# Kernel tuning notes

Measured on AMD Instinct MI355X. Metric: run time of the kernel, lower is better.

Reference implementation:

```python
import jax, jax.numpy as jnp
import numpy as np

HIDDEN, NOISE, MLPW, NCOND, DATA, INIT_NOISE = 64, 16, 128, 4, 8, 16
T, B = 128, 8192
TSCALE = 1.0


def _lipswish(x):
    return 0.909 * x * jax.nn.sigmoid(x)


def _mlp(x, Ws, bs):
    for W, b in zip(Ws[:-1], bs[:-1]):
        x = _lipswish(x @ W + b)
    return TSCALE * jnp.tanh(x @ Ws[-1] + bs[-1])  # tanh regularization, tscale=1.0


def setup_inputs():
    key = jax.random.key(0)
    ks = jax.random.split(key, 12)

    def lin(k, fi, fo):
        k1, k2 = jax.random.split(k)
        lim = 1.0 / float(np.sqrt(fi))
        W = jax.random.uniform(k1, (fi, fo), minval=-lim, maxval=lim, dtype=jnp.float32)
        b = jax.random.uniform(k2, (fo,), minval=-lim, maxval=lim, dtype=jnp.float32)
        return W, b

    ind = 1 + HIDDEN + NCOND  # cat([t, x, c0])
    dr_W0, dr_b0 = lin(ks[0], ind, MLPW)
    dr_W1, dr_b1 = lin(ks[1], MLPW, MLPW)
    dr_W2, dr_b2 = lin(ks[2], MLPW, HIDDEN)
    di_W0, di_b0 = lin(ks[3], ind, MLPW)
    di_W1, di_b1 = lin(ks[4], MLPW, MLPW)
    di_W2, di_b2 = lin(ks[5], MLPW, HIDDEN * NOISE)
    init_W, init_b = lin(ks[6], INIT_NOISE + NCOND, HIDDEN)
    ro_W, ro_b = lin(ks[7], HIDDEN + NCOND, DATA)

    ts = jnp.linspace(0.0, 1.0, T, dtype=jnp.float32)
    dt = 1.0 / (T - 1)
    dW = jax.random.normal(ks[8], (T - 1, B, NOISE), dtype=jnp.float32) * float(np.sqrt(dt))
    conditions = jax.random.normal(ks[9], (NCOND,), dtype=jnp.float32)
    return dict(ts=ts, conditions=conditions, dW=dW,
                dr_W0=dr_W0, dr_b0=dr_b0, dr_W1=dr_W1, dr_b1=dr_b1, dr_W2=dr_W2, dr_b2=dr_b2,
                di_W0=di_W0, di_b0=di_b0, di_W1=di_W1, di_b1=di_b1, di_W2=di_W2, di_b2=di_b2,
                init_W=init_W, init_b=init_b, ro_W=ro_W, ro_b=ro_b, batch_size=B)


def reference(ts, conditions, dW, dr_W0, dr_b0, dr_W1, dr_b1, dr_W2, dr_b2,
              di_W0, di_b0, di_W1, di_b1, di_W2, di_b2, init_W, init_b, ro_W, ro_b,
              batch_size):
    drWs, drbs = (dr_W0, dr_W1, dr_W2), (dr_b0, dr_b1, dr_b2)
    diWs, dibs = (di_W0, di_W1, di_W2), (di_b0, di_b1, di_b2)

    h0 = jnp.ones((batch_size, INIT_NOISE), jnp.float32)  # fixed=True initial point
    c0 = jnp.broadcast_to(conditions[None, :], (batch_size, NCOND))
    x0 = jnp.concatenate([h0, c0], 1) @ init_W + init_b  # (B, H)

    def fg(t, x):
        tcol = jnp.full((x.shape[0], 1), t, x.dtype)
        tx = jnp.concatenate([tcol, x, c0], 1)
        f = _mlp(tx, drWs, drbs)  # (B, H)
        g = _mlp(tx, diWs, dibs).reshape(x.shape[0], HIDDEN, NOISE)  # (B, H, M)
        return f, g

    f0, g0 = fg(ts[0], x0)
    dts = jnp.diff(ts)

    def step(carry, inp):
        y, z, fz, gz = carry
        t1, dt, dw = inp
        # reversible Heun (Stratonovich): auxiliary state z, re-used (f,g) at (t_n, z_n)
        z1 = 2.0 * y - z + fz * dt + jnp.einsum('bhm,bm->bh', gz, dw)
        f1, g1 = fg(t1, z1)
        y1 = y + 0.5 * dt * (fz + f1) + 0.5 * jnp.einsum('bhm,bm->bh', gz + g1, dw)
        return (y1, z1, f1, g1), y1

    _, ys = jax.lax.scan(step, (x0, x0, f0, g0), (ts[1:], dts, dW))
    xs = jnp.concatenate([x0[None], ys], 0).transpose(1, 0, 2)  # (B, T, H)
    nT = xs.shape[1]
    cs = jnp.broadcast_to(c0[:, None, :], (batch_size, nT, NCOND))
    out = jnp.concatenate([xs, cs], -1) @ ro_W + ro_b  # (B, T, data)
    ts_e = jnp.broadcast_to(ts[None, :, None], (batch_size, nT, 1))
    # linear_interpolation_coeffs with no NaNs is the identity on the values
    return jnp.concatenate([ts_e, out], -1)  # (B, T, 1 + data)
```

## Files before the change

kernel.cpp:

```cpp
#include <hip/hip_runtime.h>
#include <hip/hip_bf16.h>
#include <cstdint>
#include <cstddef>

#define B_TOT   8192
#define T_TOT   128
#define ROWS    32
#define THREADS 1024

typedef __bf16 bf16x8 __attribute__((ext_vector_type(8)));
typedef float  f32x4  __attribute__((ext_vector_type(4)));

#define WSF_X0    0
#define WSF_BCD   64
#define WSF_BCG   192
#define WSF_ROB   320
#define WSB_SMALL 1536
#define WSB_WD2   (WSB_SMALL + 49152*2)
#define WSB_WG2   (WSB_WD2 + 8192*2)
#define WSB_ROWP  (WSB_WG2 + 131072*2)
#define WSB_TOTAL (WSB_ROWP + 1024*2)

__device__ __forceinline__ unsigned short f2bf(float v){
  union { float f; unsigned u; } x; x.f = v;
  unsigned r = (x.u + 0x7FFFu + ((x.u >> 16) & 1u)) >> 16;
  return (unsigned short)r;
}
__device__ __forceinline__ unsigned cvtpk(float lo, float hi){
  unsigned r;
  asm("v_cvt_pk_bf16_f32 %0, %1, %2" : "=v"(r) : "v"(lo), "v"(hi));
  return r;
}
__device__ __forceinline__ float fexp2(float x){ return __builtin_amdgcn_exp2f(x); }
__device__ __forceinline__ float frcp (float x){ return __builtin_amdgcn_rcpf(x); }
__device__ __forceinline__ float swishf(float x){
  float e = fexp2(-1.44269504088896340f * x);
  return x * frcp(1.0f + e);
}
__device__ __forceinline__ float tanhfast(float x){
  float e = fexp2(2.88539008177792681f * x);
  return 1.0f - 2.0f * frcp(e + 1.0f);
}
__device__ __forceinline__ f32x4 mfma16(bf16x8 a, bf16x8 b, f32x4 c){
  return __builtin_amdgcn_mfma_f32_16x16x32_bf16(a, b, c, 0, 0, 0);
}

__global__ void prep_kernel(const float* __restrict__ cond,
    const float* __restrict__ drW0, const float* __restrict__ drb0,
    const float* __restrict__ drW1, const float* __restrict__ drW2,
    const float* __restrict__ diW0, const float* __restrict__ dib0,
    const float* __restrict__ diW1, const float* __restrict__ diW2,
    const float* __restrict__ initW, const float* __restrict__ initb,
    const float* __restrict__ roW,  const float* __restrict__ rob,
    char* __restrict__ ws)
{
  float* wsf = (float*)ws;
  unsigned short* wsm = (unsigned short*)(ws + WSB_SMALL);
  unsigned short* wd2 = (unsigned short*)(ws + WSB_WD2);
  unsigned short* wg2 = (unsigned short*)(ws + WSB_WG2);
  unsigned short* rwp = (unsigned short*)(ws + WSB_ROWP);
  int tid = blockIdx.x * blockDim.x + threadIdx.x;
  int nth = gridDim.x * blockDim.x;

  for (int h = tid; h < 64; h += nth){
    float s = initb[h];
    #pragma unroll
    for (int i = 0; i < 16; i++) s += initW[i*64 + h];
    #pragma unroll
    for (int c = 0; c < 4; c++) s += cond[c] * initW[(16+c)*64 + h];
    wsf[WSF_X0 + h] = s;
  }
  for (int j = tid; j < 128; j += nth){
    float sd = drb0[j], sg = dib0[j];
    #pragma unroll
    for (int c = 0; c < 4; c++){
      sd += cond[c] * drW0[(65+c)*128 + j];
      sg += cond[c] * diW0[(65+c)*128 + j];
    }
    wsf[WSF_BCD + j] = sd; wsf[WSF_BCG + j] = sg;
  }
  for (int d = tid; d < 8; d += nth){
    float s = rob[d];
    #pragma unroll
    for (int c = 0; c < 4; c++) s += cond[c] * roW[(64+c)*8 + d];
    wsf[WSF_ROB + d] = s;
  }
  for (int u = tid; u < 49152; u += nth){
    int j = u & 7, lane = (u >> 3) & 63, frag = u >> 9;
    int k8 = ((lane >> 4) << 3) + j, o16 = lane & 15;
    float v;
    if (frag < 16)      { int kc = frag & 1,      ot = frag >> 1;      v = drW0[(1 + kc*32 + k8)*128 + ot*16 + o16]; }
    else if (frag < 48) { int f = frag - 16; int kc = f & 3, ot = f >> 2; v = 0.909f * drW1[(kc*32 + k8)*128 + ot*16 + o16]; }
    else if (frag < 64) { int f = frag - 48; int kc = f & 1, ot = f >> 1; v = diW0[(1 + kc*32 + k8)*128 + ot*16 + o16]; }
    else                { int f = frag - 64; int kc = f & 3, ot = f >> 2; v = 0.909f * diW1[(kc*32 + k8)*128 + ot*16 + o16]; }
    wsm[u] = f2bf(v);
  }
  for (int u = tid; u < 8192; u += nth){
    int j = u & 7, lane = (u >> 3) & 63, frag = u >> 9, kc = frag & 3, ot = frag >> 2;
    wd2[u] = f2bf(0.909f * drW2[(kc*32 + ((lane>>4)<<3) + j)*64 + ot*16 + (lane & 15)]);
  }
  for (int u = tid; u < 131072; u += nth){
    int j = u & 7, lane = (u >> 3) & 63, frag = u >> 9, kc = frag & 3, ot = frag >> 2;
    wg2[u] = f2bf(0.909f * diW2[(kc*32 + ((lane>>4)<<3) + j)*1024 + ot*16 + (lane & 15)]);
  }
  for (int u = tid; u < 1024; u += nth){
    int j = u & 7, lane = (u >> 3) & 63, kc = u >> 9;
    int k = kc*32 + ((lane>>4)<<3) + j, o = lane & 15;
    rwp[u] = (o < 8) ? f2bf(roW[k*8 + o]) : (unsigned short)0;
  }
}

__global__ __launch_bounds__(THREADS) void sde_kernel(
    const float* __restrict__ dW,  const float* __restrict__ tsg,
    const float* __restrict__ drW0, const float* __restrict__ diW0,
    const float* __restrict__ bd1, const float* __restrict__ bg1,
    const float* __restrict__ bd2, const float* __restrict__ bg2,
    const char* __restrict__ ws, float* __restrict__ out)
{
  __shared__ unsigned short smallW[49152];
  __shared__ unsigned short z1buf[2048];
  __shared__ unsigned short ybuf[2048];
  __shared__ unsigned short h1d[4096];
  __shared__ unsigned short h1g[4096];
  __shared__ unsigned short h2d[4096];
  __shared__ unsigned short h2g[4096];
  __shared__ float f1T[2048];
  __shared__ float tsbuf[128];
  __shared__ float bcdS[128], bcgS[128];
  __shared__ float wtdS[128], wtgS[128];
  __shared__ float bd1S[128], bg1S[128];
  __shared__ float bd2S[64];
  __shared__ float bg2S[1024];
  __shared__ float dwcS[640], dwnS[640];
  __shared__ float robiasS[8];

  const float* wsf = (const float*)ws;
  const unsigned short* wsSmall = (const unsigned short*)(ws + WSB_SMALL);
  const unsigned short* wsWd2   = (const unsigned short*)(ws + WSB_WD2);
  const unsigned short* wsWg2   = (const unsigned short*)(ws + WSB_WG2);
  const unsigned short* wsRoWp  = (const unsigned short*)(ws + WSB_ROWP);

  const int tid = threadIdx.x;
  const int w  = tid >> 6;
  const int l  = tid & 63;
  const int lg = l >> 4;
  const int li = l & 15;
  const int p  = w >> 3;
  const int ot = w & 7;
  const int B0 = blockIdx.x * ROWS;
  const int row = tid >> 5;
  const int h0  = (tid & 31) << 1;

  const int aEven = lg*512 + ((li ^ lg) << 4);
  const int aOdd  = aEven ^ 64;
  const int gW    = (ot*2 + (lg>>1)) & 7;
  const int wOff  = (ot*2 + (lg>>1))*512 + ((li ^ gW) << 4) + ((lg & 1) << 3);
  const int gZ    = h0 >> 3;
  const int zOff  = gZ*512 + ((row ^ (gZ & 7)) << 4) + ((h0 & 7) << 1);
  const int dOff  = li*80 + lg*16;
  const int sOff1 = (p ? 49152 : 0)     + ot*2048 + l*16;
  const int sOff2 = (p ? 65536 : 16384) + ot*4096 + l*16;
  const int upd0  = h0*32 + (row ^ (h0 & 31));
  const int upd1  = (h0+1)*32 + (row ^ ((h0+1) & 31));
  const int otD   = (w - 8) >> 1, bmD = (w - 8) & 1;

  {
    const uint4* src = (const uint4*)wsSmall;
    uint4* dst = (uint4*)smallW;
    for (int i = tid; i < 6144; i += THREADS) dst[i] = src[i];
    for (int i = tid; i < 128; i += THREADS){
      tsbuf[i] = tsg[i];
      bcdS[i] = wsf[WSF_BCD + i]; bcgS[i] = wsf[WSF_BCG + i];
      wtdS[i] = drW0[i];          wtgS[i] = diW0[i];
      bd1S[i] = bd1[i];           bg1S[i] = bg1[i];
    }
    for (int i = tid; i < 1024; i += THREADS) bg2S[i] = bg2[i];
    if (tid < 64) bd2S[tid] = bd2[tid];
    if (tid < 8) robiasS[tid] = wsf[WSF_ROB + tid];
  }

  float y[2], z[2], fz[2], az[2];
  #pragma unroll
  for (int j = 0; j < 2; j++){ float v = wsf[WSF_X0 + h0 + j]; y[j] = v; z[j] = v; }

  auto writeZ = [&](){ *(unsigned*)((char*)z1buf + zOff) = cvtpk(z[0], z[1]); };
  auto writeY = [&](){ *(unsigned*)((char*)ybuf  + zOff) = cvtpk(y[0], y[1]); };
  writeZ(); writeY();

  __syncthreads();

  auto rdfrag = [&](const unsigned short* buf, int kc, int bm) -> bf16x8 {
    int off = ((kc & 1) ? aOdd : aEven) + kc*2048 + bm*256;
    return *(const bf16x8*)((const char*)buf + off);
  };

  auto OUTPROJ = [&](int tcur){
    f32x4 acc = {0.f,0.f,0.f,0.f};
    #pragma unroll
    for (int kc = 0; kc < 2; kc++){
      bf16x8 rw = *(const bf16x8*)((const char*)wsRoWp + kc*1024 + l*16);
      acc = mfma16(rw, rdfrag(ybuf, kc, w), acc);
    }
    const int brow = w*16 + li;
    float* orow = out + (size_t)(B0 + brow)*1152 + (size_t)tcur*9;
    if (lg < 2){
      #pragma unroll
      for (int r = 0; r < 4; r++) orow[1 + lg*4 + r] = acc[r] + robiasS[lg*4 + r];
    } else if (lg == 2){
      orow[0] = tsbuf[tcur];
    }
  };

  auto PIPE = [&](float tval, int kdwc, int kdwn, int tcur){
    if (tid < 256){
      const float* src = dW + ((tid < 128) ? (size_t)kdwc : (size_t)kdwn)*131072
                            + (size_t)B0*16;
      float* dst = (tid < 128) ? dwcS : dwnS;
      int i = tid & 127;
      *(f32x4*)(dst + (i>>2)*20 + (i&3)*4) = *(const f32x4*)(src + i*4);
    }
    {
      f32x4 acc0 = {0.f,0.f,0.f,0.f}, acc1 = {0.f,0.f,0.f,0.f};
      #pragma unroll
      for (int kc = 0; kc < 2; kc++){
        bf16x8 af = *(const bf16x8*)((const char*)smallW + sOff1 + kc*1024);
        acc0 = mfma16(af, rdfrag(z1buf, kc, 0), acc0);
        acc1 = mfma16(af, rdfrag(z1buf, kc, 1), acc1);
      }
      f32x4 bcv = *(const f32x4*)((p ? bcgS : bcdS) + ot*16 + lg*4);
      f32x4 wtv = *(const f32x4*)((p ? wtgS : wtdS) + ot*16 + lg*4);
      unsigned short* hout = p ? h1g : h1d;
      #pragma unroll
      for (int bm = 0; bm < 2; bm++){
        const f32x4& acc = bm ? acc1 : acc0;
        float xx[4];
        #pragma unroll
        for (int r = 0; r < 4; r++) xx[r] = swishf(acc[r] + bcv[r] + tval*wtv[r]);
        uint2 v; v.x = cvtpk(xx[0], xx[1]); v.y = cvtpk(xx[2], xx[3]);
        *(uint2*)((char*)hout + wOff + bm*256) = v;
      }
    }
    __syncthreads();
    {
      const unsigned short* hin  = p ? h1g : h1d;
      unsigned short*       hout = p ? h2g : h2d;
      f32x4 acc0 = {0.f,0.f,0.f,0.f}, acc1 = {0.f,0.f,0.f,0.f};
      #pragma unroll
      for (int kc = 0; kc < 4; kc++){
        bf16x8 af = *(const bf16x8*)((const char*)smallW + sOff2 + kc*1024);
        acc0 = mfma16(af, rdfrag(hin, kc, 0), acc0);
        acc1 = mfma16(af, rdfrag(hin, kc, 1), acc1);
      }
      f32x4 b1v = *(const f32x4*)((p ? bg1S : bd1S) + ot*16 + lg*4);
      #pragma unroll
      for (int bm = 0; bm < 2; bm++){
        const f32x4& acc = bm ? acc1 : acc0;
        float xx[4];
        #pragma unroll
        for (int r = 0; r < 4; r++) xx[r] = swishf(acc[r] + b1v[r]);
        uint2 v; v.x = cvtpk(xx[0], xx[1]); v.y = cvtpk(xx[2], xx[3]);
        *(uint2*)((char*)hout + wOff + bm*256) = v;
      }
    }
    __syncthreads();
    {
      float* bT = (float*)h1d;
      float* aT = (float*)h1g;
      bf16x8 gf[2][4];
      #pragma unroll
      for (int kc = 0; kc < 4; kc++){
        gf[0][kc] = rdfrag(h2g, kc, 0);
        gf[1][kc] = rdfrag(h2g, kc, 1);
      }
      if (w >= 8){
        f32x4 acc = {0.f,0.f,0.f,0.f};
        #pragma unroll
        for (int kc = 0; kc < 4; kc++){
          bf16x8 wf = *(const bf16x8*)((const char*)wsWd2 + otD*4096 + kc*1024 + l*16);
          acc = mfma16(wf, rdfrag(h2d, kc, bmD), acc);
        }
        f32x4 bdv = *(const f32x4*)(bd2S + otD*16 + lg*4);
        const int browD = bmD*16 + li;
        #pragma unroll
        for (int r = 0; r < 4; r++){
          int h = otD*16 + lg*4 + r;
          f1T[h*32 + (browD ^ (h & 31))] = tanhfast(acc[r] + bdv[r]);
        }
      } else if (tcur >= 0 && w < 2){
        OUTPROJ(tcur);
      }
      #pragma unroll
      for (int o = 0; o < 4; o++){
        const int h = w*4 + o;
        f32x4 acc0 = {0.f,0.f,0.f,0.f}, acc1 = {0.f,0.f,0.f,0.f};
        #pragma unroll
        for (int kc = 0; kc < 4; kc++){
          bf16x8 fk = *(const bf16x8*)((const char*)wsWg2 + (size_t)((h*4 + kc)*1024) + l*16);
          acc0 = mfma16(fk, gf[0][kc], acc0);
          acc1 = mfma16(fk, gf[1][kc], acc1);
        }
        f32x4 bgv = *(const f32x4*)(bg2S + h*16 + lg*4);
        #pragma unroll
        for (int bm = 0; bm < 2; bm++){
          const f32x4& acc = bm ? acc1 : acc0;
          f32x4 dwcv = *(const f32x4*)((const char*)dwcS + dOff + bm*1280);
          f32x4 dwnv = *(const f32x4*)((const char*)dwnS + dOff + bm*1280);
          float bs = 0.f, as_ = 0.f;
          #pragma unroll
          for (int r = 0; r < 4; r++){
            float g = tanhfast(acc[r] + bgv[r]);
            bs  += g * dwcv[r];
            as_ += g * dwnv[r];
          }
          bs  += __shfl_xor(bs, 16);  bs  += __shfl_xor(bs, 32);
          as_ += __shfl_xor(as_, 16); as_ += __shfl_xor(as_, 32);
          const int brow = bm*16 + li;
          const int idx = h*32 + (brow ^ (h & 31));
          if (lg == 0)      bT[idx] = bs;
          else if (lg == 1) aT[idx] = as_;
        }
      }
    }
  };

  PIPE(tsbuf[0], 0, 0, -1);
  __syncthreads();
  {
    #pragma unroll
    for (int j = 0; j < 2; j++){
      int idx = j ? upd1 : upd0;
      fz[j] = f1T[idx];
      az[j] = ((const float*)h1g)[idx];
    }
    float dt0 = tsbuf[1] - tsbuf[0];
    #pragma unroll
    for (int j = 0; j < 2; j++) z[j] = 2.f*y[j] - z[j] + fz[j]*dt0 + az[j];
    writeZ();
  }
  __syncthreads();

  for (int k = 0; k < 127; k++){
    PIPE(tsbuf[k+1], k, (k < 126) ? (k+1) : 126, k);
    __syncthreads();
    float f1[2], bb[2], an[2];
    #pragma unroll
    for (int j = 0; j < 2; j++){
      int idx = j ? upd1 : upd0;
      f1[j] = f1T[idx];
      bb[j] = ((const float*)h1d)[idx];
      an[j] = ((const float*)h1g)[idx];
    }
    float dtk = tsbuf[k+1] - tsbuf[k];
    #pragma unroll
    for (int j = 0; j < 2; j++){
      y[j] += 0.5f*dtk*(fz[j] + f1[j]) + 0.5f*(az[j] + bb[j]);
      fz[j] = f1[j]; az[j] = an[j];
    }
    writeY();
    if (k < 126){
      float dtn = tsbuf[k+2] - tsbuf[k+1];
      #pragma unroll
      for (int j = 0; j < 2; j++) z[j] = 2.f*y[j] - z[j] + fz[j]*dtn + az[j];
      writeZ();
    }
    __syncthreads();
  }

  if (w < 2) OUTPROJ(127);
}

extern "C" void kernel_launch(void* const* d_in, const int* in_sizes, int n_in,
                              void* d_out, int out_size, void* d_ws, size_t ws_size,
                              hipStream_t stream)
{
  const float* ts   = (const float*)d_in[0];
  const float* cond = (const float*)d_in[1];
  const float* dW   = (const float*)d_in[2];
  const float* drW0 = (const float*)d_in[3];
  const float* drb0 = (const float*)d_in[4];
  const float* drW1 = (const float*)d_in[5];
  const float* drb1 = (const float*)d_in[6];
  const float* drW2 = (const float*)d_in[7];
  const float* drb2 = (const float*)d_in[8];
  const float* diW0 = (const float*)d_in[9];
  const float* dib0 = (const float*)d_in[10];
  const float* diW1 = (const float*)d_in[11];
  const float* dib1 = (const float*)d_in[12];
  const float* diW2 = (const float*)d_in[13];
  const float* dib2 = (const float*)d_in[14];
  const float* initW= (const float*)d_in[15];
  const float* initb= (const float*)d_in[16];
  const float* roW  = (const float*)d_in[17];
  const float* rob  = (const float*)d_in[18];
  char* ws = (char*)d_ws;
  if (ws_size < (size_t)WSB_TOTAL) return;

  prep_kernel<<<dim3(256), dim3(256), 0, stream>>>(
      cond, drW0, drb0, drW1, drW2, diW0, dib0, diW1, diW2,
      initW, initb, roW, rob, ws);
  sde_kernel<<<dim3(256), dim3(THREADS), 0, stream>>>(
      dW, ts, drW0, diW0, drb1, dib1, drb2, dib2, ws, (float*)d_out);
}
```

Measured before the change: 1.024 ms.

## Halve rows per block, double grid, stream layer-2 weights from global

Each block now handles 16 batch rows with 512 threads, and the grid grows to 512 blocks. Each wave computes both the drift and diffusion MLP for one output tile, so the per-row-block MFMA pairs go away. To cut LDS use, only the first-layer weights stay in shared memory. The second-layer weights are read straight from the global workspace, and the readout weights are moved into LDS. The aim is to fill more CUs, 512 blocks against 256 on MI355X, and to allow several blocks per CU. The costs are more global/L2 weight traffic per step, weight loads amortised over fewer rows per MFMA, and an odd ldspad buffer that looks like it is there to force occupancy.

```diff
diff --git a/kernel.cpp b/kernel.cpp
--- a/kernel.cpp
+++ b/kernel.cpp
@@ -5,8 +5,9 @@
 
 #define B_TOT   8192
 #define T_TOT   128
-#define ROWS    32
-#define THREADS 1024
+#define ROWS    16
+#define THREADS 512
+#define GRID    512
 
 typedef __bf16 bf16x8 __attribute__((ext_vector_type(8)));
 typedef float  f32x4  __attribute__((ext_vector_type(4)));
@@ -110,29 +111,31 @@
   }
 }
 
-__global__ __launch_bounds__(THREADS) void sde_kernel(
+__global__ __launch_bounds__(THREADS, 4) void sde_kernel(
     const float* __restrict__ dW,  const float* __restrict__ tsg,
     const float* __restrict__ drW0, const float* __restrict__ diW0,
     const float* __restrict__ bd1, const float* __restrict__ bg1,
     const float* __restrict__ bd2, const float* __restrict__ bg2,
     const char* __restrict__ ws, float* __restrict__ out)
 {
-  __shared__ unsigned short smallW[49152];
-  __shared__ unsigned short z1buf[2048];
-  __shared__ unsigned short ybuf[2048];
-  __shared__ unsigned short h1d[4096];
-  __shared__ unsigned short h1g[4096];
-  __shared__ unsigned short h2d[4096];
-  __shared__ unsigned short h2g[4096];
-  __shared__ float f1T[2048];
+  __shared__ unsigned short smallW[16384];
+  __shared__ unsigned short roWS[1024];
+  __shared__ unsigned short z1buf[1024];
+  __shared__ unsigned short ybuf[1024];
+  __shared__ unsigned short h1d[2048];
+  __shared__ unsigned short h1g[2048];
+  __shared__ unsigned short h2d[2048];
+  __shared__ unsigned short h2g[2048];
+  __shared__ float f1T[1024];
   __shared__ float tsbuf[128];
   __shared__ float bcdS[128], bcgS[128];
   __shared__ float wtdS[128], wtgS[128];
   __shared__ float bd1S[128], bg1S[128];
   __shared__ float bd2S[64];
   __shared__ float bg2S[1024];
-  __shared__ float dwcS[640], dwnS[640];
+  __shared__ float dwcS[320], dwnS[320];
   __shared__ float robiasS[8];
+  __shared__ float ldspad[2048];
 
   const float* wsf = (const float*)ws;
   const unsigned short* wsSmall = (const unsigned short*)(ws + WSB_SMALL);
@@ -145,29 +148,29 @@
   const int l  = tid & 63;
   const int lg = l >> 4;
   const int li = l & 15;
-  const int p  = w >> 3;
-  const int ot = w & 7;
+  const int ot = w;
   const int B0 = blockIdx.x * ROWS;
   const int row = tid >> 5;
   const int h0  = (tid & 31) << 1;
 
-  const int aEven = lg*512 + ((li ^ lg) << 4);
+  const int aEven = lg*256 + ((li ^ lg) << 4);
   const int aOdd  = aEven ^ 64;
   const int gW    = (ot*2 + (lg>>1)) & 7;
-  const int wOff  = (ot*2 + (lg>>1))*512 + ((li ^ gW) << 4) + ((lg & 1) << 3);
+  const int wOff  = (ot*2 + (lg>>1))*256 + ((li ^ gW) << 4) + ((lg & 1) << 3);
   const int gZ    = h0 >> 3;
-  const int zOff  = gZ*512 + ((row ^ (gZ & 7)) << 4) + ((h0 & 7) << 1);
+  const int zOff  = gZ*256 + ((row ^ (gZ & 7)) << 4) + ((h0 & 7) << 1);
   const int dOff  = li*80 + lg*16;
-  const int sOff1 = (p ? 49152 : 0)     + ot*2048 + l*16;
-  const int sOff2 = (p ? 65536 : 16384) + ot*4096 + l*16;
-  const int upd0  = h0*32 + (row ^ (h0 & 31));
-  const int upd1  = (h0+1)*32 + (row ^ ((h0+1) & 31));
-  const int otD   = (w - 8) >> 1, bmD = (w - 8) & 1;
+  const int upd0  = h0*16 + (row ^ (h0 & 15));
+  const int upd1  = (h0+1)*16 + (row ^ ((h0+1) & 15));
 
   {
     const uint4* src = (const uint4*)wsSmall;
     uint4* dst = (uint4*)smallW;
-    for (int i = tid; i < 6144; i += THREADS) dst[i] = src[i];
+    for (int i = tid; i < 2048; i += THREADS)
+      dst[i] = src[(i < 1024) ? i : (i + 2048)];
+    const uint4* rsrc = (const uint4*)wsRoWp;
+    uint4* rdst = (uint4*)roWS;
+    for (int i = tid; i < 128; i += THREADS) rdst[i] = rsrc[i];
     for (int i = tid; i < 128; i += THREADS){
       tsbuf[i] = tsg[i];
       bcdS[i] = wsf[WSF_BCD + i]; bcgS[i] = wsf[WSF_BCG + i];
@@ -177,6 +180,7 @@
     for (int i = tid; i < 1024; i += THREADS) bg2S[i] = bg2[i];
     if (tid < 64) bd2S[tid] = bd2[tid];
     if (tid < 8) robiasS[tid] = wsf[WSF_ROB + tid];
+    if (tid == 0) ldspad[0] = 0.f;
   }
 
   float y[2], z[2], fz[2], az[2];
@@ -189,8 +193,8 @@
 
   __syncthreads();
 
-  auto rdfrag = [&](const unsigned short* buf, int kc, int bm) -> bf16x8 {
-    int off = ((kc & 1) ? aOdd : aEven) + kc*2048 + bm*256;
+  auto rdfrag = [&](const unsigned short* buf, int kc) -> bf16x8 {
+    int off = ((kc & 1) ? aOdd : aEven) + kc*1024;
     return *(const bf16x8*)((const char*)buf + off);
   };
 
@@ -198,11 +202,10 @@
     f32x4 acc = {0.f,0.f,0.f,0.f};
     #pragma unroll
     for (int kc = 0; kc < 2; kc++){
-      bf16x8 rw = *(const bf16x8*)((const char*)wsRoWp + kc*1024 + l*16);
-      acc = mfma16(rw, rdfrag(ybuf, kc, w), acc);
-    }
-    const int brow = w*16 + li;
-    float* orow = out + (size_t)(B0 + brow)*1152 + (size_t)tcur*9;
+      bf16x8 rw = *(const bf16x8*)((const char*)roWS + kc*1024 + l*16);
+      acc = mfma16(rw, rdfrag(ybuf, kc), acc);
+    }
+    float* orow = out + (size_t)(B0 + li)*1152 + (size_t)tcur*9;
     if (lg < 2){
       #pragma unroll
       for (int r = 0; r < 4; r++) orow[1 + lg*4 + r] = acc[r] + robiasS[lg*4 + r];
@@ -212,113 +215,103 @@
   };
 
   auto PIPE = [&](float tval, int kdwc, int kdwn, int tcur){
-    if (tid < 256){
-      const float* src = dW + ((tid < 128) ? (size_t)kdwc : (size_t)kdwn)*131072
+    if (tid < 128){
+      const float* src = dW + ((tid < 64) ? (size_t)kdwc : (size_t)kdwn)*131072
                             + (size_t)B0*16;
-      float* dst = (tid < 128) ? dwcS : dwnS;
-      int i = tid & 127;
+      float* dst = (tid < 64) ? dwcS : dwnS;
+      int i = tid & 63;
       *(f32x4*)(dst + (i>>2)*20 + (i&3)*4) = *(const f32x4*)(src + i*4);
     }
     {
-      f32x4 acc0 = {0.f,0.f,0.f,0.f}, acc1 = {0.f,0.f,0.f,0.f};
+      f32x4 accD = {0.f,0.f,0.f,0.f}, accG = {0.f,0.f,0.f,0.f};
       #pragma unroll
       for (int kc = 0; kc < 2; kc++){
-        bf16x8 af = *(const bf16x8*)((const char*)smallW + sOff1 + kc*1024);
-        acc0 = mfma16(af, rdfrag(z1buf, kc, 0), acc0);
-        acc1 = mfma16(af, rdfrag(z1buf, kc, 1), acc1);
-      }
-      f32x4 bcv = *(const f32x4*)((p ? bcgS : bcdS) + ot*16 + lg*4);
-      f32x4 wtv = *(const f32x4*)((p ? wtgS : wtdS) + ot*16 + lg*4);
-      unsigned short* hout = p ? h1g : h1d;
-      #pragma unroll
-      for (int bm = 0; bm < 2; bm++){
-        const f32x4& acc = bm ? acc1 : acc0;
+        bf16x8 afD = *(const bf16x8*)((const char*)smallW +         ot*2048 + kc*1024 + l*16);
+        bf16x8 afG = *(const bf16x8*)((const char*)smallW + 16384 + ot*2048 + kc*1024 + l*16);
+        bf16x8 zb  = rdfrag(z1buf, kc);
+        accD = mfma16(afD, zb, accD);
+        accG = mfma16(afG, zb, accG);
+      }
+      #pragma unroll
+      for (int p = 0; p < 2; p++){
+        const f32x4& acc = p ? accG : accD;
+        f32x4 bcv = *(const f32x4*)((p ? bcgS : bcdS) + ot*16 + lg*4);
+        f32x4 wtv = *(const f32x4*)((p ? wtgS : wtdS) + ot*16 + lg*4);
         float xx[4];
         #pragma unroll
         for (int r = 0; r < 4; r++) xx[r] = swishf(acc[r] + bcv[r] + tval*wtv[r]);
         uint2 v; v.x = cvtpk(xx[0], xx[1]); v.y = cvtpk(xx[2], xx[3]);
-        *(uint2*)((char*)hout + wOff + bm*256) = v;
+        *(uint2*)((char*)(p ? h1g : h1d) + wOff) = v;
       }
     }
     __syncthreads();
     {
-      const unsigned short* hin  = p ? h1g : h1d;
-      unsigned short*       hout = p ? h2g : h2d;
-      f32x4 acc0 = {0.f,0.f,0.f,0.f}, acc1 = {0.f,0.f,0.f,0.f};
+      f32x4 accD = {0.f,0.f,0.f,0.f}, accG = {0.f,0.f,0.f,0.f};
       #pragma unroll
       for (int kc = 0; kc < 4; kc++){
-        bf16x8 af = *(const bf16x8*)((const char*)smallW + sOff2 + kc*1024);
-        acc0 = mfma16(af, rdfrag(hin, kc, 0), acc0);
-        acc1 = mfma16(af, rdfrag(hin, kc, 1), acc1);
-      }
-      f32x4 b1v = *(const f32x4*)((p ? bg1S : bd1S) + ot*16 + lg*4);
-      #pragma unroll
-      for (int bm = 0; bm < 2; bm++){
-        const f32x4& acc = bm ? acc1 : acc0;
+        bf16x8 afD = *(const bf16x8*)((const char*)wsSmall + 16384 + ot*4096 + kc*1024 + l*16);
+        bf16x8 afG = *(const bf16x8*)((const char*)wsSmall + 65536 + ot*4096 + kc*1024 + l*16);
+        accD = mfma16(afD, rdfrag(h1d, kc), accD);
+        accG = mfma16(afG, rdfrag(h1g, kc), accG);
+      }
+      #pragma unroll
+      for (int p = 0; p < 2; p++){
+        const f32x4& acc = p ? accG : accD;
+        f32x4 b1v = *(const f32x4*)((p ? bg1S : bd1S) + ot*16 + lg*4);
         float xx[4];
         #pragma unroll
         for (int r = 0; r < 4; r++) xx[r] = swishf(acc[r] + b1v[r]);
         uint2 v; v.x = cvtpk(xx[0], xx[1]); v.y = cvtpk(xx[2], xx[3]);
-        *(uint2*)((char*)hout + wOff + bm*256) = v;
+        *(uint2*)((char*)(p ? h2g : h2d) + wOff) = v;
       }
     }
     __syncthreads();
     {
       float* bT = (float*)h1d;
       float* aT = (float*)h1g;
-      bf16x8 gf[2][4];
-      #pragma unroll
-      for (int kc = 0; kc < 4; kc++){
-        gf[0][kc] = rdfrag(h2g, kc, 0);
-        gf[1][kc] = rdfrag(h2g, kc, 1);
-      }
-      if (w >= 8){
+      bf16x8 gf[4];
+      #pragma unroll
+      for (int kc = 0; kc < 4; kc++) gf[kc] = rdfrag(h2g, kc);
+      if (w < 4){
         f32x4 acc = {0.f,0.f,0.f,0.f};
         #pragma unroll
         for (int kc = 0; kc < 4; kc++){
-          bf16x8 wf = *(const bf16x8*)((const char*)wsWd2 + otD*4096 + kc*1024 + l*16);
-          acc = mfma16(wf, rdfrag(h2d, kc, bmD), acc);
+          bf16x8 wf = *(const bf16x8*)((const char*)wsWd2 + w*4096 + kc*1024 + l*16);
+          acc = mfma16(wf, rdfrag(h2d, kc), acc);
         }
-        f32x4 bdv = *(const f32x4*)(bd2S + otD*16 + lg*4);
-        const int browD = bmD*16 + li;
+        f32x4 bdv = *(const f32x4*)(bd2S + w*16 + lg*4);
         #pragma unroll
         for (int r = 0; r < 4; r++){
-          int h = otD*16 + lg*4 + r;
-          f1T[h*32 + (browD ^ (h & 31))] = tanhfast(acc[r] + bdv[r]);
+          int h = w*16 + lg*4 + r;
+          f1T[h*16 + (li ^ (h & 15))] = tanhfast(acc[r] + bdv[r]);
         }
-      } else if (tcur >= 0 && w < 2){
+      } else if (w == 4 && tcur >= 0){
         OUTPROJ(tcur);
       }
       #pragma unroll
-      for (int o = 0; o < 4; o++){
-        const int h = w*4 + o;
-        f32x4 acc0 = {0.f,0.f,0.f,0.f}, acc1 = {0.f,0.f,0.f,0.f};
+      for (int o = 0; o < 8; o++){
+        const int h = w*8 + o;
+        f32x4 acc = {0.f,0.f,0.f,0.f};
         #pragma unroll
         for (int kc = 0; kc < 4; kc++){
           bf16x8 fk = *(const bf16x8*)((const char*)wsWg2 + (size_t)((h*4 + kc)*1024) + l*16);
-          acc0 = mfma16(fk, gf[0][kc], acc0);
-          acc1 = mfma16(fk, gf[1][kc], acc1);
+          acc = mfma16(fk, gf[kc], acc);
         }
         f32x4 bgv = *(const f32x4*)(bg2S + h*16 + lg*4);
-        #pragma unroll
-        for (int bm = 0; bm < 2; bm++){
-          const f32x4& acc = bm ? acc1 : acc0;
-          f32x4 dwcv = *(const f32x4*)((const char*)dwcS + dOff + bm*1280);
-          f32x4 dwnv = *(const f32x4*)((const char*)dwnS + dOff + bm*1280);
-          float bs = 0.f, as_ = 0.f;
-          #pragma unroll
-          for (int r = 0; r < 4; r++){
-            float g = tanhfast(acc[r] + bgv[r]);
-            bs  += g * dwcv[r];
-            as_ += g * dwnv[r];
-          }
-          bs  += __shfl_xor(bs, 16);  bs  += __shfl_xor(bs, 32);
-          as_ += __shfl_xor(as_, 16); as_ += __shfl_xor(as_, 32);
-          const int brow = bm*16 + li;
-          const int idx = h*32 + (brow ^ (h & 31));
-          if (lg == 0)      bT[idx] = bs;
-          else if (lg == 1) aT[idx] = as_;
+        f32x4 dwcv = *(const f32x4*)((const char*)dwcS + dOff);
+        f32x4 dwnv = *(const f32x4*)((const char*)dwnS + dOff);
+        float bs = 0.f, as_ = 0.f;
+        #pragma unroll
+        for (int r = 0; r < 4; r++){
+          float g = tanhfast(acc[r] + bgv[r]);
+          bs  += g * dwcv[r];
+          as_ += g * dwnv[r];
         }
+        bs  += __shfl_xor(bs, 16);  bs  += __shfl_xor(bs, 32);
+        as_ += __shfl_xor(as_, 16); as_ += __shfl_xor(as_, 32);
+        const int idx = h*16 + (li ^ (h & 15));
+        if (lg == 0)      bT[idx] = bs;
+        else if (lg == 1) aT[idx] = as_;
       }
     }
   };
@@ -366,7 +359,7 @@
     __syncthreads();
   }
 
-  if (w < 2) OUTPROJ(127);
+  if (w == 4) OUTPROJ(127);
 }
 
 extern "C" void kernel_launch(void* const* d_in, const int* in_sizes, int n_in,
@@ -398,6 +391,6 @@
   prep_kernel<<<dim3(256), dim3(256), 0, stream>>>(
       cond, drW0, drb0, drW1, drW2, diW0, dib0, diW1, diW2,
       initW, initb, roW, rob, ws);
-  sde_kernel<<<dim3(256), dim3(THREADS), 0, stream>>>(
+  sde_kernel<<<dim3(GRID), dim3(THREADS), 0, stream>>>(
       dW, ts, drW0, diW0, drb1, dib1, drb2, dib2, ws, (float*)d_out);
 }
```

Result: slower. 1.077 ms (+5.2%).
